# Performance work log

Hardware: AMD Instinct MI355X
Metric: run time of the kernel (lower is better)

## Reference

```python
import jax, jax.numpy as jnp
import numpy as np

D_MODEL = 1024
NHEAD = 16
HEAD_DIM = D_MODEL // NHEAD
MAX_LEN = 4096
ROPE_BASE = 500.0


def _rope_tables(L, dim):
    inv_freq = 1.0 / (ROPE_BASE ** (jnp.arange(0, dim, 2, dtype=jnp.float32) / dim))
    t = jnp.arange(L, dtype=jnp.float32)
    freqs = jnp.einsum('i,j->ij', t, inv_freq)  # [L, dim/2]
    emb = jnp.concatenate([freqs, freqs], axis=-1)  # [L, dim]
    return jnp.cos(emb), jnp.sin(emb)


def _rotate_half(x):
    x1, x2 = jnp.split(x, 2, axis=-1)
    return jnp.concatenate([-x2, x1], axis=-1)


def _apply_rope(x, cos, sin):
    return x * cos + _rotate_half(x) * sin


def setup_inputs() -> dict:
    key = jax.random.key(0)
    ks = jax.random.split(key, 6)
    B, L = 4, 2048
    bound_qkv = 1.0 / np.sqrt(D_MODEL)
    x = jax.random.normal(ks[0], (B, L, D_MODEL), dtype=jnp.float32)
    key_padding_mask = jnp.zeros((B, L), dtype=bool)
    W_qkv = jax.random.uniform(ks[1], (3 * D_MODEL, D_MODEL), jnp.float32, -bound_qkv, bound_qkv)
    b_qkv = jax.random.uniform(ks[2], (3 * D_MODEL,), jnp.float32, -bound_qkv, bound_qkv)
    W_out = jax.random.uniform(ks[3], (D_MODEL, D_MODEL), jnp.float32, -bound_qkv, bound_qkv)
    b_out = jax.random.uniform(ks[4], (D_MODEL,), jnp.float32, -bound_qkv, bound_qkv)
    return {"x": x, "key_padding_mask": key_padding_mask,
            "W_qkv": W_qkv, "b_qkv": b_qkv, "W_out": W_out, "b_out": b_out}


def reference(x, key_padding_mask, W_qkv, b_qkv, W_out, b_out):
    B, L, D = x.shape
    H, hd = NHEAD, HEAD_DIM
    qkv = x @ W_qkv.T + b_qkv  # [B, L, 3D]
    q, k, v = jnp.split(qkv, 3, axis=-1)
    # [B, H, L, hd]
    q = q.reshape(B, L, H, hd).transpose(0, 2, 1, 3)
    k = k.reshape(B, L, H, hd).transpose(0, 2, 1, 3)
    v = v.reshape(B, L, H, hd).transpose(0, 2, 1, 3)
    cos, sin = _rope_tables(L, hd)  # [L, hd]
    q = _apply_rope(q, cos, sin)
    k = _apply_rope(k, cos, sin)
    scores = jnp.einsum('bhqd,bhkd->bhqk', q, k) / jnp.sqrt(jnp.float32(hd))
    mask = key_padding_mask[:, None, None, :]  # [B,1,1,L]
    scores = jnp.where(mask, -jnp.inf, scores)
    attn = jax.nn.softmax(scores, axis=-1)
    out = jnp.einsum('bhqk,bhkd->bhqd', attn, v)
    out = out.transpose(0, 2, 1, 3).reshape(B, L, D)
    return out @ W_out.T + b_out
```

## Files before the change

kernel.cpp:

```cpp
#include <hip/hip_runtime.h>
#include <stdint.h>

typedef __attribute__((ext_vector_type(8))) __bf16 bf16x8;
typedef __attribute__((ext_vector_type(4))) short short4v;
typedef __attribute__((ext_vector_type(4))) float f32x4;

#if __has_builtin(__builtin_amdgcn_exp2f)
#define EXP2(x) __builtin_amdgcn_exp2f(x)
#else
#define EXP2(x) exp2f(x)
#endif

__device__ __forceinline__ short f2bf(float f) {
  union { float f; uint32_t u; } v; v.f = f;
  uint32_t r = (v.u + 0x7fffu + ((v.u >> 16) & 1u)) >> 16;
  return (short)(uint16_t)r;
}

__device__ __forceinline__ uint32_t pk2bf(float a, float b) {
  union { __bf16 h; uint16_t u; } x, y;
  x.h = (__bf16)a; y.h = (__bf16)b;
  return (uint32_t)x.u | ((uint32_t)y.u << 16);
}

__device__ __forceinline__ void gl2lds16(const void* g, const void* lds) {
  __builtin_amdgcn_global_load_lds(
      (const __attribute__((address_space(1))) void*)(uintptr_t)g,
      (__attribute__((address_space(3))) void*)(uint32_t)(uintptr_t)lds,
      16, 0, 0);
}

__device__ __forceinline__ bf16x8 frag8(const short* p) {
  return *(const bf16x8*)(const void*)p;
}

__global__ void convert3_k(const float* __restrict__ s0, short* __restrict__ d0, int n0,
                           const float* __restrict__ s1, short* __restrict__ d1, int n1,
                           const float* __restrict__ s2, short* __restrict__ d2, int n2) {
  int i = blockIdx.x * blockDim.x + threadIdx.x;
  int t0 = n0 >> 2, t1 = t0 + (n1 >> 2), t2 = t1 + (n2 >> 2);
  const float* s; short* d; int off;
  if (i < t0) { s = s0; d = d0; off = i; }
  else if (i < t1) { s = s1; d = d1; off = i - t0; }
  else if (i < t2) { s = s2; d = d2; off = i - t1; }
  else return;
  float4 v = ((const float4*)s)[off];
  short4v o;
  o.x = f2bf(v.x); o.y = f2bf(v.y); o.z = f2bf(v.z); o.w = f2bf(v.w);
  *(short4v*)(d + off * 4) = o;
}

__global__ void rope_tab_k(float* __restrict__ cosT, float* __restrict__ sinT,
                           const unsigned char* __restrict__ mask, float* __restrict__ maskf) {
  int i = blockIdx.x * blockDim.x + threadIdx.x;
  int pos = i >> 5, j = i & 31;
  float invf = exp2f(-(float)j * (8.965784284662087f / 32.0f));
  float ang = (float)pos * invf;
  float s, c;
  sincosf(ang, &s, &c);
  cosT[i] = c; sinT[i] = s;
  if (i < 8192) maskf[i] = mask[i] ? -1e30f : 0.0f;
}

template <int EPI>
__global__ __launch_bounds__(256, 3)
void gemm_bt_k(const short* __restrict__ A, const short* __restrict__ Bm,
               const float* __restrict__ bias, int N, int K,
               float* __restrict__ Cout,
               const float* __restrict__ cosT, const float* __restrict__ sinT,
               short* __restrict__ Qb, short* __restrict__ Kb, short* __restrict__ Vt) {
  __shared__ short As[2][128 * 32];
  __shared__ short Bs[2][128 * 32];
  const int tid = threadIdx.x;
  const int lane = tid & 63;
  const int w = tid >> 6;
  const int g = lane >> 4, l15 = lane & 15;
  const int wm = (w >> 1) * 64, wn = (w & 1) * 64;
  const int bm = blockIdx.x, bn = blockIdx.y;

  const int rseg = lane >> 2;
  const int cofs = ((lane & 3) ^ ((lane >> 3) & 3)) * 8;
  const int sA0 = w, sA1 = w + 4;
  const int arow0 = (bm * 128 + sA0 * 16 + rseg) * K;
  const int arow1 = (bm * 128 + sA1 * 16 + rseg) * K;
  const int brow0 = (bn * 128 + sA0 * 16 + rseg) * K;
  const int brow1 = (bn * 128 + sA1 * 16 + rseg) * K;

  const int rsw = (l15 >> 1) & 3;

  f32x4 acc[4][4];
#pragma unroll
  for (int i = 0; i < 4; i++)
#pragma unroll
    for (int j = 0; j < 4; j++) acc[i][j] = f32x4{0.f, 0.f, 0.f, 0.f};

  gl2lds16(A + arow0 + cofs, &As[0][sA0 * 512]);
  gl2lds16(A + arow1 + cofs, &As[0][sA1 * 512]);
  gl2lds16(Bm + brow0 + cofs, &Bs[0][sA0 * 512]);
  gl2lds16(Bm + brow1 + cofs, &Bs[0][sA1 * 512]);

  int cur = 0;
  for (int k0 = 0; k0 < K; k0 += 32, cur ^= 1) {
    __syncthreads();
    int nxt = cur ^ 1;
    int k1 = k0 + 32;
    if (k1 < K) {
      gl2lds16(A + arow0 + k1 + cofs, &As[nxt][sA0 * 512]);
      gl2lds16(A + arow1 + k1 + cofs, &As[nxt][sA1 * 512]);
      gl2lds16(Bm + brow0 + k1 + cofs, &Bs[nxt][sA0 * 512]);
      gl2lds16(Bm + brow1 + k1 + cofs, &Bs[nxt][sA1 * 512]);
    }
    bf16x8 af[4], bf[4];
#pragma unroll
    for (int im = 0; im < 4; im++) af[im] = frag8(&As[cur][(wm + im * 16 + l15) * 32 + (g ^ rsw) * 8]);
#pragma unroll
    for (int jn = 0; jn < 4; jn++) bf[jn] = frag8(&Bs[cur][(wn + jn * 16 + l15) * 32 + (g ^ rsw) * 8]);
#pragma unroll
    for (int im = 0; im < 4; im++)
#pragma unroll
      for (int jn = 0; jn < 4; jn++)
        acc[im][jn] = __builtin_amdgcn_mfma_f32_16x16x32_bf16(af[im], bf[jn], acc[im][jn], 0, 0, 0);
  }

  const int row0 = bm * 128 + wm + g * 4;
  const int col0 = bn * 128 + wn;

  if (EPI == 0) {
#pragma unroll
    for (int jn = 0; jn < 4; jn++) {
      float bb = bias[col0 + jn * 16 + l15];
#pragma unroll
      for (int im = 0; im < 4; im++)
#pragma unroll
        for (int r = 0; r < 4; r++) {
          int row = row0 + im * 16 + r;
          Cout[row * N + col0 + jn * 16 + l15] = acc[im][jn][r] + bb;
        }
    }
  } else {
#pragma unroll
    for (int jn = 0; jn < 4; jn++) {
      float bb = bias[col0 + jn * 16 + l15];
#pragma unroll
      for (int im = 0; im < 4; im++)
#pragma unroll
        for (int r = 0; r < 4; r++) acc[im][jn][r] += bb;
    }
    const int sector = col0 >> 10;
    const int h = (col0 & 1023) >> 6;
    if (sector == 2) {
#pragma unroll
      for (int jn = 0; jn < 4; jn++) {
        int d = jn * 16 + l15;
#pragma unroll
        for (int im = 0; im < 4; im++) {
          int row = row0 + im * 16;
          int b = row >> 11, pos = row & 2047;
          union { uint32_t u[2]; short4v s4; } pw;
          pw.u[0] = pk2bf(acc[im][jn][0], acc[im][jn][1]);
          pw.u[1] = pk2bf(acc[im][jn][2], acc[im][jn][3]);
          *(short4v*)&Vt[((b * 16 + h) * 64 + d) * 2048 + pos] = pw.s4;
        }
      }
    } else {
      short* dst = (sector == 0) ? Qb : Kb;
      const float scl = (sector == 0) ? 0.18033688011112042f : 1.0f;
#pragma unroll
      for (int jn = 0; jn < 4; jn++) {
        int d = jn * 16 + l15;
        int j = d & 31;
#pragma unroll
        for (int im = 0; im < 4; im++)
#pragma unroll
          for (int r = 0; r < 4; r++) {
            int row = row0 + im * 16 + r;
            int b = row >> 11, pos = row & 2047;
            float c = cosT[pos * 32 + j];
            float s = sinT[pos * 32 + j];
            float xv = acc[im][jn][r];
            float xp = acc[im][jn ^ 2][r];
            float rot = (jn < 2) ? -xp : xp;
            dst[((b * 16 + h) * 2048 + pos) * 64 + d] = f2bf((xv * c + rot * s) * scl);
          }
      }
    }
  }
}

__global__ __launch_bounds__(256, 3)
void attn_k(const short* __restrict__ Qb, const short* __restrict__ Kb,
            const short* __restrict__ Vt, const float* __restrict__ maskf,
            short* __restrict__ attn) {
  __shared__ short Ks[2][64 * 64];
  __shared__ short Vs[2][64 * 64];
  __shared__ short Ps[4][32 * 64];
  const int tid = threadIdx.x, lane = tid & 63, w = tid >> 6;
  const int g = lane >> 4, l15 = lane & 15;
  const int sw = l15 & 7;
  const int qt = blockIdx.x, bh = blockIdx.y;
  const int b = bh >> 4, h = bh & 15;

  bf16x8 aq[2][2];
#pragma unroll
  for (int qi = 0; qi < 2; qi++)
#pragma unroll
    for (int kc = 0; kc < 2; kc++) {
      int q = qt * 128 + w * 32 + qi * 16 + l15;
      aq[qi][kc] = *(const bf16x8*)(const void*)(Qb + (bh * 2048 + q) * 64 + kc * 32 + g * 8);
    }
  bf16x8 aone;
#pragma unroll
  for (int i = 0; i < 8; i++) aone[i] = (__bf16)1.0f;

  f32x4 o[4][2];
#pragma unroll
  for (int jd = 0; jd < 4; jd++)
#pragma unroll
    for (int qi = 0; qi < 2; qi++) o[jd][qi] = f32x4{0.f, 0.f, 0.f, 0.f};
  f32x4 lacc[2] = {f32x4{0.f, 0.f, 0.f, 0.f}, f32x4{0.f, 0.f, 0.f, 0.f}};

  const float* mfp = maskf + b * 2048;
  const int r8 = lane >> 3;
  const int cst = (lane & 7) ^ r8;
  const int t0s = w * 4;

#pragma unroll
  for (int t = 0; t < 4; t++) {
    int s = t0s + t;
    if (s < 8) gl2lds16(Kb + (bh * 2048 + s * 8 + r8) * 64 + cst * 8, &Ks[0][s * 512]);
    else       gl2lds16(Vt + (bh * 64 + (s - 8) * 8 + r8) * 2048 + cst * 8, &Vs[0][(s - 8) * 512]);
  }

  int cur = 0;
  for (int kt = 0; kt < 32; kt++, cur ^= 1) {
    const int kbase = kt * 64;
    __syncthreads();
    int nxt = cur ^ 1;
    if (kt + 1 < 32) {
      const int nb = kbase + 64;
#pragma unroll
      for (int t = 0; t < 4; t++) {
        int s = t0s + t;
        if (s < 8) gl2lds16(Kb + (bh * 2048 + nb + s * 8 + r8) * 64 + cst * 8, &Ks[nxt][s * 512]);
        else       gl2lds16(Vt + (bh * 64 + (s - 8) * 8 + r8) * 2048 + nb + cst * 8, &Vs[nxt][(s - 8) * 512]);
      }
    }

    f32x4 sv[4][2];
#pragma unroll
    for (int kvt = 0; kvt < 4; kvt++) {
      f32x4 mf = *(const f32x4*)(mfp + kbase + kvt * 16 + g * 4);
      sv[kvt][0] = mf; sv[kvt][1] = mf;
    }
#pragma unroll
    for (int kvt = 0; kvt < 4; kvt++)
#pragma unroll
      for (int kc = 0; kc < 2; kc++) {
        bf16x8 ak = frag8(&Ks[cur][(kvt * 16 + l15) * 64 + ((kc * 4 + g) ^ sw) * 8]);
        sv[kvt][0] = __builtin_amdgcn_mfma_f32_16x16x32_bf16(ak, aq[0][kc], sv[kvt][0], 0, 0, 0);
        sv[kvt][1] = __builtin_amdgcn_mfma_f32_16x16x32_bf16(ak, aq[1][kc], sv[kvt][1], 0, 0, 0);
      }

#pragma unroll
    for (int qi = 0; qi < 2; qi++)
#pragma unroll
      for (int kvt = 0; kvt < 4; kvt++) {
        union { uint32_t u[2]; short4v s4; } pw;
        pw.u[0] = pk2bf(EXP2(sv[kvt][qi][0]), EXP2(sv[kvt][qi][1]));
        pw.u[1] = pk2bf(EXP2(sv[kvt][qi][2]), EXP2(sv[kvt][qi][3]));
        *(short4v*)&Ps[w][(qi * 16 + l15) * 64 + ((2 * kvt + (g >> 1)) ^ sw) * 8 + (g & 1) * 4] = pw.s4;
      }

#pragma unroll
    for (int kc = 0; kc < 2; kc++) {
      bf16x8 av[4];
#pragma unroll
      for (int jd = 0; jd < 4; jd++)
        av[jd] = frag8(&Vs[cur][(jd * 16 + l15) * 64 + ((kc * 4 + g) ^ sw) * 8]);
#pragma unroll
      for (int qi = 0; qi < 2; qi++) {
        bf16x8 bp = frag8(&Ps[w][(qi * 16 + l15) * 64 + ((kc * 4 + g) ^ sw) * 8]);
#pragma unroll
        for (int jd = 0; jd < 4; jd++)
          o[jd][qi] = __builtin_amdgcn_mfma_f32_16x16x32_bf16(av[jd], bp, o[jd][qi], 0, 0, 0);
        lacc[qi] = __builtin_amdgcn_mfma_f32_16x16x32_bf16(aone, bp, lacc[qi], 0, 0, 0);
      }
    }
  }

#pragma unroll
  for (int qi = 0; qi < 2; qi++) {
    float inv = 1.0f / lacc[qi][0];
    int q = qt * 128 + w * 32 + qi * 16 + l15;
#pragma unroll
    for (int jd = 0; jd < 4; jd++) {
      union { uint32_t u[2]; short4v s4; } pw;
      pw.u[0] = pk2bf(o[jd][qi][0] * inv, o[jd][qi][1] * inv);
      pw.u[1] = pk2bf(o[jd][qi][2] * inv, o[jd][qi][3] * inv);
      *(short4v*)&attn[(b * 2048 + q) * 1024 + h * 64 + jd * 16 + g * 4] = pw.s4;
    }
  }
}

extern "C" void kernel_launch(void* const* d_in, const int* in_sizes, int n_in,
                              void* d_out, int out_size, void* d_ws, size_t ws_size,
                              hipStream_t stream) {
  const float* x = (const float*)d_in[0];
  const unsigned char* mask = (const unsigned char*)d_in[1];
  const float* W_qkv = (const float*)d_in[2];
  const float* b_qkv = (const float*)d_in[3];
  const float* W_out = (const float*)d_in[4];
  const float* b_out = (const float*)d_in[5];
  float* out = (float*)d_out;

  char* ws = (char*)d_ws;
  short* xb    = (short*)(ws + 0);
  short* wqkvb = (short*)(ws + 16777216);
  short* woutb = (short*)(ws + 23068672);
  float* cosT  = (float*)(ws + 25165824);
  float* sinT  = (float*)(ws + 25427968);
  short* Qb    = (short*)(ws + 25690112);
  short* Kb    = (short*)(ws + 42467328);
  short* Vtb   = (short*)(ws + 59244544);
  short* attnb = (short*)(ws + 76021760);
  float* maskf = (float*)(ws + 92798976);

  convert3_k<<<12288, 256, 0, stream>>>(x, xb, 8388608, W_qkv, wqkvb, 3145728, W_out, woutb, 1048576);
  rope_tab_k<<<256, 256, 0, stream>>>(cosT, sinT, mask, maskf);
  gemm_bt_k<1><<<dim3(64, 24), 256, 0, stream>>>(xb, wqkvb, b_qkv, 3072, 1024,
                                                 nullptr, cosT, sinT, Qb, Kb, Vtb);
  attn_k<<<dim3(16, 64), 256, 0, stream>>>(Qb, Kb, Vtb, maskf, attnb);
  gemm_bt_k<0><<<dim3(64, 8), 256, 0, stream>>>(attnb, woutb, b_out, 1024, 1024,
                                                out, nullptr, nullptr, nullptr, nullptr, nullptr);
}
```

Before: 304.3 us.

## Shrink attention blocks to two waves with 32-key tiles and new LDS swizzle

Restructures the attention kernel from 4-wave blocks over 128 queries with 64-key tiles to 2-wave blocks over 64 queries with 32-key tiles. The grid doubles, K and V loading is split between the two waves, and the V/P LDS layouts get a new 4-way swizzle. The aim is higher occupancy and smaller shared-memory use per block. In exchange, each K/V tile is reused by half as many queries, so global K/V traffic doubles, and the loop has twice as many iterations and barriers.

```diff
diff --git a/kernel.cpp b/kernel.cpp
--- a/kernel.cpp
+++ b/kernel.cpp
@@ -187,16 +187,17 @@
   }
 }
 
-__global__ __launch_bounds__(256, 3)
+__global__ __launch_bounds__(128, 4)
 void attn_k(const short* __restrict__ Qb, const short* __restrict__ Kb,
             const short* __restrict__ Vt, const float* __restrict__ maskf,
             short* __restrict__ attn) {
-  __shared__ short Ks[2][64 * 64];
-  __shared__ short Vs[2][64 * 64];
-  __shared__ short Ps[4][32 * 64];
+  __shared__ short Ks[2][32 * 64];
+  __shared__ short Vs[2][64 * 32];
+  __shared__ short Ps[2][32 * 32];
   const int tid = threadIdx.x, lane = tid & 63, w = tid >> 6;
   const int g = lane >> 4, l15 = lane & 15;
-  const int sw = l15 & 7;
+  const int swk = l15 & 7;
+  const int fv = (l15 ^ (l15 >> 2)) & 3;
   const int qt = blockIdx.x, bh = blockIdx.y;
   const int b = bh >> 4, h = bh & 15;
 
@@ -205,7 +206,7 @@
   for (int qi = 0; qi < 2; qi++)
 #pragma unroll
     for (int kc = 0; kc < 2; kc++) {
-      int q = qt * 128 + w * 32 + qi * 16 + l15;
+      int q = qt * 64 + w * 32 + qi * 16 + l15;
       aq[qi][kc] = *(const bf16x8*)(const void*)(Qb + (bh * 2048 + q) * 64 + kc * 32 + g * 8);
     }
   bf16x8 aone;
@@ -220,43 +221,51 @@
   f32x4 lacc[2] = {f32x4{0.f, 0.f, 0.f, 0.f}, f32x4{0.f, 0.f, 0.f, 0.f}};
 
   const float* mfp = maskf + b * 2048;
-  const int r8 = lane >> 3;
-  const int cst = (lane & 7) ^ r8;
-  const int t0s = w * 4;
-
-#pragma unroll
-  for (int t = 0; t < 4; t++) {
-    int s = t0s + t;
-    if (s < 8) gl2lds16(Kb + (bh * 2048 + s * 8 + r8) * 64 + cst * 8, &Ks[0][s * 512]);
-    else       gl2lds16(Vt + (bh * 64 + (s - 8) * 8 + r8) * 2048 + cst * 8, &Vs[0][(s - 8) * 512]);
+
+  const int kr8 = lane >> 3;
+  const int kcst = (lane & 7) ^ kr8;
+  const int vrs = lane >> 2;
+  const int vcs = (lane & 3) ^ ((vrs ^ (vrs >> 2)) & 3);
+
+  if (w == 0) {
+#pragma unroll
+    for (int s = 0; s < 4; s++)
+      gl2lds16(Kb + (bh * 2048 + s * 8 + kr8) * 64 + kcst * 8, &Ks[0][s * 512]);
+  } else {
+#pragma unroll
+    for (int s = 0; s < 4; s++)
+      gl2lds16(Vt + (bh * 64 + s * 16 + vrs) * 2048 + vcs * 8, &Vs[0][s * 512]);
   }
 
   int cur = 0;
-  for (int kt = 0; kt < 32; kt++, cur ^= 1) {
-    const int kbase = kt * 64;
+  for (int kt = 0; kt < 64; kt++, cur ^= 1) {
+    const int kbase = kt * 32;
     __syncthreads();
     int nxt = cur ^ 1;
-    if (kt + 1 < 32) {
-      const int nb = kbase + 64;
-#pragma unroll
-      for (int t = 0; t < 4; t++) {
-        int s = t0s + t;
-        if (s < 8) gl2lds16(Kb + (bh * 2048 + nb + s * 8 + r8) * 64 + cst * 8, &Ks[nxt][s * 512]);
-        else       gl2lds16(Vt + (bh * 64 + (s - 8) * 8 + r8) * 2048 + nb + cst * 8, &Vs[nxt][(s - 8) * 512]);
-      }
-    }
-
-    f32x4 sv[4][2];
-#pragma unroll
-    for (int kvt = 0; kvt < 4; kvt++) {
+    if (kt + 1 < 64) {
+      const int nb = kbase + 32;
+      if (w == 0) {
+#pragma unroll
+        for (int s = 0; s < 4; s++)
+          gl2lds16(Kb + (bh * 2048 + nb + s * 8 + kr8) * 64 + kcst * 8, &Ks[nxt][s * 512]);
+      } else {
+#pragma unroll
+        for (int s = 0; s < 4; s++)
+          gl2lds16(Vt + (bh * 64 + s * 16 + vrs) * 2048 + nb + vcs * 8, &Vs[nxt][s * 512]);
+      }
+    }
+
+    f32x4 sv[2][2];
+#pragma unroll
+    for (int kvt = 0; kvt < 2; kvt++) {
       f32x4 mf = *(const f32x4*)(mfp + kbase + kvt * 16 + g * 4);
       sv[kvt][0] = mf; sv[kvt][1] = mf;
     }
 #pragma unroll
-    for (int kvt = 0; kvt < 4; kvt++)
+    for (int kvt = 0; kvt < 2; kvt++)
 #pragma unroll
       for (int kc = 0; kc < 2; kc++) {
-        bf16x8 ak = frag8(&Ks[cur][(kvt * 16 + l15) * 64 + ((kc * 4 + g) ^ sw) * 8]);
+        bf16x8 ak = frag8(&Ks[cur][(kvt * 16 + l15) * 64 + ((kc * 4 + g) ^ swk) * 8]);
         sv[kvt][0] = __builtin_amdgcn_mfma_f32_16x16x32_bf16(ak, aq[0][kc], sv[kvt][0], 0, 0, 0);
         sv[kvt][1] = __builtin_amdgcn_mfma_f32_16x16x32_bf16(ak, aq[1][kc], sv[kvt][1], 0, 0, 0);
       }
@@ -264,22 +273,21 @@
 #pragma unroll
     for (int qi = 0; qi < 2; qi++)
 #pragma unroll
-      for (int kvt = 0; kvt < 4; kvt++) {
+      for (int kvt = 0; kvt < 2; kvt++) {
         union { uint32_t u[2]; short4v s4; } pw;
         pw.u[0] = pk2bf(EXP2(sv[kvt][qi][0]), EXP2(sv[kvt][qi][1]));
         pw.u[1] = pk2bf(EXP2(sv[kvt][qi][2]), EXP2(sv[kvt][qi][3]));
-        *(short4v*)&Ps[w][(qi * 16 + l15) * 64 + ((2 * kvt + (g >> 1)) ^ sw) * 8 + (g & 1) * 4] = pw.s4;
-      }
-
-#pragma unroll
-    for (int kc = 0; kc < 2; kc++) {
+        *(short4v*)&Ps[w][(qi * 16 + l15) * 32 + (((kvt * 2 + (g >> 1)) ^ fv) * 8) + (g & 1) * 4] = pw.s4;
+      }
+
+    {
       bf16x8 av[4];
 #pragma unroll
       for (int jd = 0; jd < 4; jd++)
-        av[jd] = frag8(&Vs[cur][(jd * 16 + l15) * 64 + ((kc * 4 + g) ^ sw) * 8]);
+        av[jd] = frag8(&Vs[cur][(jd * 16 + l15) * 32 + (g ^ fv) * 8]);
 #pragma unroll
       for (int qi = 0; qi < 2; qi++) {
-        bf16x8 bp = frag8(&Ps[w][(qi * 16 + l15) * 64 + ((kc * 4 + g) ^ sw) * 8]);
+        bf16x8 bp = frag8(&Ps[w][(qi * 16 + l15) * 32 + (g ^ fv) * 8]);
 #pragma unroll
         for (int jd = 0; jd < 4; jd++)
           o[jd][qi] = __builtin_amdgcn_mfma_f32_16x16x32_bf16(av[jd], bp, o[jd][qi], 0, 0, 0);
@@ -291,7 +299,7 @@
 #pragma unroll
   for (int qi = 0; qi < 2; qi++) {
     float inv = 1.0f / lacc[qi][0];
-    int q = qt * 128 + w * 32 + qi * 16 + l15;
+    int q = qt * 64 + w * 32 + qi * 16 + l15;
 #pragma unroll
     for (int jd = 0; jd < 4; jd++) {
       union { uint32_t u[2]; short4v s4; } pw;
@@ -329,7 +337,7 @@
   rope_tab_k<<<256, 256, 0, stream>>>(cosT, sinT, mask, maskf);
   gemm_bt_k<1><<<dim3(64, 24), 256, 0, stream>>>(xb, wqkvb, b_qkv, 3072, 1024,
                                                  nullptr, cosT, sinT, Qb, Kb, Vtb);
-  attn_k<<<dim3(16, 64), 256, 0, stream>>>(Qb, Kb, Vtb, maskf, attnb);
+  attn_k<<<dim3(32, 64), 128, 0, stream>>>(Qb, Kb, Vtb, maskf, attnb);
   gemm_bt_k<0><<<dim3(64, 8), 256, 0, stream>>>(attnb, woutb, b_out, 1024, 1024,
                                                 out, nullptr, nullptr, nullptr, nullptr, nullptr);
 }
```

New measurement: 293.9 us. 1.04x faster.
